# Kernel tuning notes

Measured on AMD Instinct MI355X. Metric: run time of the kernel, lower is better.

## Reference

```python
import jax, jax.numpy as jnp
import numpy as np

B, H, W, R, C = 4, 64, 64, 64, 32  # batch, height, width, in-channels r, conv out-channels


def setup_inputs() -> dict:
    key = jax.random.key(0)
    kx, kf, kg = jax.random.split(key, 3)
    x = jax.random.normal(kx, (B, H, W, R), dtype=jnp.float32)
    # 1x1 conv with in_channels=1: kernel is effectively a length-C vector
    w_f = jax.random.normal(kf, (C,), dtype=jnp.float32) * 0.1
    w_g = jax.random.normal(kg, (C,), dtype=jnp.float32) * 0.1
    gamma = jnp.ones((), dtype=jnp.float32)
    return {"x": x, "w_f": w_f, "w_g": w_g, "gamma": gamma}


def reference(x, w_f, w_g, gamma):
    b, h, w, r = x.shape
    hw = h * w
    xs = x.reshape(b, hw, r)                      # [B, HW, R]
    # conv_f / conv_g: each scalar of xs times weight vector -> [B, HW, R*C]
    x_f = (xs[..., None] * w_f).reshape(b, hw, -1)
    x_g = (xs[..., None] * w_g).reshape(b, hw, -1)
    attn = jnp.einsum('bik,bjk->bij', x_f, x_g)   # [B, HW, HW]
    attn = jax.nn.softmax(attn, axis=-1) * gamma
    # out[b,j,r] = sum_i attn[b,j,i] * xs[b,i,r]
    out = jnp.einsum('bji,bir->bjr', attn, xs)
    return out.reshape(b, h, w, r)
```

## Files before the change

### kernel.cpp

```cpp
#include <hip/hip_runtime.h>


#define N_SEQ 4096
#define LOG2E 1.4426950408889634f

typedef __attribute__((ext_vector_type(8))) short short8;
typedef __attribute__((ext_vector_type(4))) short short4v;
typedef __attribute__((ext_vector_type(4))) float f4;
typedef __attribute__((ext_vector_type(16))) float f32x16;
typedef _Float16 half8  __attribute__((ext_vector_type(8)));
typedef _Float16 half2t __attribute__((ext_vector_type(2)));
typedef __fp16   fp16x2 __attribute__((ext_vector_type(2)));

union U8  { short8 v8; short4v v4[2]; unsigned short u[8]; };
union PKU { fp16x2 f; half2t h; unsigned int u; };
union US  { short8 s; half8 h; };
union W4U { unsigned int u[4]; half8 h; };

#define MFMA16(a,b,c)  __builtin_amdgcn_mfma_f32_16x16x32_bf16(a,b,c,0,0,0)
#define MFMA32F(a,b,c) __builtin_amdgcn_mfma_f32_32x32x16_f16(a,b,c,0,0,0)

static __device__ __forceinline__ unsigned short f2bf(float f){
  unsigned int u = __float_as_uint(f);
  u += 0x7fffu + ((u>>16)&1u);
  return (unsigned short)(u>>16);
}
static __device__ __forceinline__ float bf2f(unsigned short b){
  return __uint_as_float(((unsigned int)b)<<16);
}
static __device__ __forceinline__ unsigned int pk_u32(float a, float b){
#if __has_builtin(__builtin_amdgcn_cvt_pkrtz)
  PKU u; u.f = __builtin_amdgcn_cvt_pkrtz(a, b); return u.u;
#else
  PKU u; u.h.x = (_Float16)a; u.h.y = (_Float16)b; return u.u;
#endif
}
static __device__ __forceinline__ float fexp2(float x){
#if __has_builtin(__builtin_amdgcn_exp2f)
  return __builtin_amdgcn_exp2f(x);
#else
  return exp2f(x);
#endif
}
static __device__ __forceinline__ f4 splat4(float v){ f4 r; r.x=v; r.y=v; r.z=v; r.w=v; return r; }
static __device__ __forceinline__ f4 exp2v(f4 v){
  f4 r; r.x=fexp2(v.x); r.y=fexp2(v.y); r.z=fexp2(v.z); r.w=fexp2(v.w); return r;
}
static __device__ __forceinline__ f4 max4(f4 a, f4 b){
  f4 r; r.x=fmaxf(a.x,b.x); r.y=fmaxf(a.y,b.y); r.z=fmaxf(a.z,b.z); r.w=fmaxf(a.w,b.w); return r;
}
static __device__ __forceinline__ f4 shx4(f4 v, int m){
  f4 r; r.x=__shfl_xor(v.x,m,64); r.y=__shfl_xor(v.y,m,64);
        r.z=__shfl_xor(v.z,m,64); r.w=__shfl_xor(v.w,m,64); return r;
}
static __device__ __forceinline__ f32x16 zero16(){
  f32x16 z;
  #pragma unroll
  for (int i = 0; i < 16; ++i) z[i] = 0.f;
  return z;
}
static __device__ __forceinline__ void gload16(const unsigned short* g, unsigned short* l){
  __builtin_amdgcn_global_load_lds((const __attribute__((address_space(1))) void*)g,
                                   (__attribute__((address_space(3))) void*)l, 16, 0, 0);
}
static __device__ __forceinline__ half8 mkfrag(unsigned int Da0, unsigned int Da1,
                                               unsigned int Db0, unsigned int Db1, bool hib){
  const unsigned int e0 = __shfl_xor(hib ? Da0 : Db0, 32, 64);
  const unsigned int e1 = __shfl_xor(hib ? Da1 : Db1, 32, 64);
  W4U w;
  w.u[0] = hib ? e0  : Da0;
  w.u[1] = hib ? e1  : Da1;
  w.u[2] = hib ? Db0 : e0;
  w.u[3] = hib ? Db1 : e1;
  return w.h;
}

__global__ __launch_bounds__(256) void prep6_kernel(
    const float* __restrict__ x,
    unsigned short* __restrict__ XF, unsigned short* __restrict__ VF)
{
  __shared__ __align__(16) unsigned short T [64][82];
  __shared__ __align__(16) unsigned short TT[64][82];
  const int tid  = threadIdx.x;
  const int bb   = blockIdx.x >> 6;
  const int tile = blockIdx.x & 63;
  {
    const int r  = tid >> 2;
    const int c4 = tid & 3;
    const float* src = x + ((size_t)(bb*N_SEQ + tile*64 + r))*64 + c4*16;
    unsigned short h[16];
    #pragma unroll
    for (int i = 0; i < 4; ++i) {
      const float4 f = *(const float4*)(src + i*4);
      const unsigned int u0 = pk_u32(f.x, f.y);
      const unsigned int u1 = pk_u32(f.z, f.w);
      h[i*4+0] = (unsigned short)(u0 & 0xffffu);
      h[i*4+1] = (unsigned short)(u0 >> 16);
      h[i*4+2] = (unsigned short)(u1 & 0xffffu);
      h[i*4+3] = (unsigned short)(u1 >> 16);
    }
    #pragma unroll
    for (int j = 0; j < 16; ++j) T[r][c4*16+j] = h[j];
    #pragma unroll
    for (int j = 0; j < 16; ++j) TT[c4*16+j][r] = h[j];
  }
  __syncthreads();
  const size_t ob = ((size_t)(bb*64 + tile)) * 4096;
  #pragma unroll
  for (int s0 = 0; s0 < 2; ++s0) {
    const int s  = s0*256 + tid;
    const int fb = s >> 6;
    const int l  = s & 63;
    const int rr = (fb >> 2)*32 + (l & 31);
    const int cc = (fb & 3)*16 + (l >> 5)*8;
    U8 a, b;
    #pragma unroll
    for (int j = 0; j < 8; ++j) { a.u[j] = T[rr][cc+j]; b.u[j] = TT[rr][cc+j]; }
    *(short8*)(XF + ob + (size_t)s*8) = a.v8;
    *(short8*)(VF + ob + (size_t)s*8) = b.v8;
  }
}

__global__ __launch_bounds__(512, 2) void fattn9_kernel(
    const float* __restrict__ wf, const float* __restrict__ wg,
    const float* __restrict__ gm,
    const unsigned short* __restrict__ XF, const unsigned short* __restrict__ VF,
    float* __restrict__ out)
{
  __shared__ __align__(16) unsigned char SMEM[66560];
  unsigned short* TLE  = (unsigned short*)SMEM;
  float*          LO   = (float*)SMEM;
  float*          LSUM = (float*)(SMEM + 65536);

  const int tid  = threadIdx.x;
  const int lane = tid & 63;
  const int wv   = tid >> 6;
  const int l31  = lane & 31;
  const int hi   = lane >> 5;
  const bool hib = hi != 0;
  const int par  = wv >> 2;
  const int kg   = (wv >> 1) & 1;
  const int qg   = wv & 1;
  const int bb   = blockIdx.x >> 6;
  const int qt   = blockIdx.x & 63;

  float s = 0.f;
  #pragma unroll
  for (int i = 0; i < 32; ++i) s += wf[i]*wg[i];
  const float s2 = s * LOG2E;
  const _Float16 s2h = (_Float16)s2;

  half8 qf[4];
  {
    const unsigned short* xq = XF + ((size_t)(bb*64 + qt))*4096 + lane*8;
    half8 sv;
    #pragma unroll
    for (int j = 0; j < 8; ++j) sv[j] = s2h;
    #pragma unroll
    for (int kst = 0; kst < 4; ++kst) {
      US u; u.s = *(const short8*)(xq + (qg*4+kst)*512);
      qf[kst] = u.h * sv;
    }
  }

  f32x16 Oc[2];
  Oc[0] = zero16(); Oc[1] = zero16();
  float lacc = 0.f;

  const unsigned short* gK = XF + (size_t)bb*64*4096;
  const unsigned short* gV = VF + (size_t)bb*64*4096;

  #define STAGE(p, b)                                                            \
    _Pragma("unroll")                                                            \
    for (int c = 0; c < 4; ++c) {                                                \
      const unsigned short* src =                                                \
        ((c >> 1) ? gV : gK) + ((size_t)((p)*2 + (c & 1)))*4096 + tid*8;         \
      unsigned short* dst = TLE + ((((b)*2 + (c & 1))*2 + (c >> 1))*4096) + tid*8;\
      gload16(src, dst);                                                         \
    }

  STAGE(0, 0);
  __syncthreads();

  #pragma unroll 1
  for (int it = 0; it < 32; ++it) {
    const int cur = it & 1;
    if (it + 1 < 32) { STAGE(it + 1, cur ^ 1); }

    const unsigned short* KB = TLE + ((cur*2 + par)*2 + 0)*4096;
    const unsigned short* VB = KB + 4096;

    half8 kf[4];
    #pragma unroll
    for (int kst = 0; kst < 4; ++kst) {
      US u; u.s = *(const short8*)(KB + ((kg*4+kst)*64 + lane)*8);
      kf[kst] = u.h;
    }
    f32x16 St = zero16();
    __builtin_amdgcn_s_setprio(1);
    #pragma unroll
    for (int kst = 0; kst < 4; ++kst) St = MFMA32F(kf[kst], qf[kst], St);
    __builtin_amdgcn_s_setprio(0);

    float p[16];
    float sm = 0.f;
    #pragma unroll
    for (int r = 0; r < 16; ++r) { p[r] = fexp2(St[r]); sm += p[r]; }
    lacc += sm;
    const unsigned int D0 = pk_u32(p[0],  p[1]);
    const unsigned int D1 = pk_u32(p[2],  p[3]);
    const unsigned int D2 = pk_u32(p[4],  p[5]);
    const unsigned int D3 = pk_u32(p[6],  p[7]);
    const unsigned int D4 = pk_u32(p[8],  p[9]);
    const unsigned int D5 = pk_u32(p[10], p[11]);
    const unsigned int D6 = pk_u32(p[12], p[13]);
    const unsigned int D7 = pk_u32(p[14], p[15]);
    half8 pa0 = mkfrag(D0, D1, D2, D3, hib);
    half8 pa1 = mkfrag(D4, D5, D6, D7, hib);

    __builtin_amdgcn_s_setprio(1);
    #pragma unroll
    for (int dg = 0; dg < 2; ++dg) {
      US v0, v1;
      v0.s = *(const short8*)(VB + ((dg*4 + kg*2 + 0)*64 + lane)*8);
      v1.s = *(const short8*)(VB + ((dg*4 + kg*2 + 1)*64 + lane)*8);
      Oc[dg] = MFMA32F(pa0, v0.h, Oc[dg]);
      Oc[dg] = MFMA32F(pa1, v1.h, Oc[dg]);
    }
    __builtin_amdgcn_s_setprio(0);

    __syncthreads();
  }

  lacc += __shfl_xor(lacc, 32, 64);

  #pragma unroll
  for (int dg = 0; dg < 2; ++dg)
    #pragma unroll
    for (int r = 0; r < 16; ++r) {
      const int ql = (r & 3) + 8*(r >> 2) + 4*hi;
      LO[wv*2048 + ql*64 + dg*32 + l31] = Oc[dg][r];
    }
  if (hi == 0) LSUM[wv*32 + l31] = lacc;
  __syncthreads();

  {
    const float gamma = gm[0];
    const int r  = tid >> 3;
    const int d0 = (tid & 7)*8;
    const int q  = r & 31;
    const int qr = r >> 5;
    const float l = LSUM[(qr+0)*32 + q] + LSUM[(qr+2)*32 + q]
                  + LSUM[(qr+4)*32 + q] + LSUM[(qr+6)*32 + q];
    const float w = gamma / l;
    float acc[8];
    #pragma unroll
    for (int j = 0; j < 8; ++j) acc[j] = 0.f;
    #pragma unroll
    for (int j = 0; j < 4; ++j) {
      const float* src = LO + (qr + j*2)*2048 + q*64 + d0;
      #pragma unroll
      for (int e = 0; e < 8; ++e) acc[e] += src[e];
    }
    float4 r0, r1;
    r0.x = acc[0]*w; r0.y = acc[1]*w; r0.z = acc[2]*w; r0.w = acc[3]*w;
    r1.x = acc[4]*w; r1.y = acc[5]*w; r1.z = acc[6]*w; r1.w = acc[7]*w;
    float* dst = out + ((size_t)(bb*N_SEQ + qt*64 + r))*64 + d0;
    *(float4*)dst = r0;
    *(float4*)(dst + 4) = r1;
  }
}

#define LDKF 72
#define TILEF (64*LDKF)
#define LDP 36

__global__ __launch_bounds__(256) void fattn_fallback(
    const float* __restrict__ x, const float* __restrict__ wf,
    const float* __restrict__ wg, const float* __restrict__ gm,
    float* __restrict__ out)
{
  __shared__ __align__(16) unsigned short KHI[2*TILEF];
  __shared__ __align__(16) unsigned short KLO[2*TILEF];
  __shared__ __align__(16) unsigned short VT [2*TILEF];
  __shared__ __align__(16) unsigned short PB [4*32*LDP];

  const int tid  = threadIdx.x;
  const int lane = tid & 63;
  const int wv   = tid >> 6;
  const int mg   = wv & 1;
  const int hh   = wv >> 1;
  const int quad = lane >> 4;
  const int l15  = lane & 15;
  const int bb   = blockIdx.x >> 6;
  const int qb   = (blockIdx.x & 63) << 6;

  float s = 0.f;
  #pragma unroll
  for (int i = 0; i < 32; ++i) s += wf[i]*wg[i];
  const float s2 = s * LOG2E;
  const float gamma = gm[0];

  const float* xb = x + ((size_t)bb * N_SEQ) * 64;

  short8 qhf[2][2], qlf[2][2];
  #pragma unroll
  for (int mt = 0; mt < 2; ++mt) {
    const int row = qb + mg*32 + mt*16 + l15;
    #pragma unroll
    for (int c = 0; c < 2; ++c) {
      const float* src = xb + row*64 + c*32 + quad*8;
      const float4 a0 = *(const float4*)src;
      const float4 a1 = *(const float4*)(src+4);
      float qv[8] = {a0.x,a0.y,a0.z,a0.w,a1.x,a1.y,a1.z,a1.w};
      U8 vh, vl;
      #pragma unroll
      for (int j = 0; j < 8; ++j) {
        float q = qv[j]*s2;
        unsigned short hb = f2bf(q);
        vh.u[j] = (short)hb;
        vl.u[j] = (short)f2bf(q - bf2f(hb));
      }
      qhf[mt][c] = vh.v8; qlf[mt][c] = vl.v8;
    }
  }

  f4 Oc[2][4], mo[2], ls[2];
  #pragma unroll
  for (int mt = 0; mt < 2; ++mt) {
    mo[mt] = splat4(-1e30f);
    ls[mt] = splat4(0.f);
    #pragma unroll
    for (int nt = 0; nt < 4; ++nt) Oc[mt][nt] = splat4(0.f);
  }

  const int sh   = tid >> 7;
  const int srow = (tid & 127) >> 1;
  const int sch  = tid & 1;

  float4 sr[8];
  {
    const float* sp = xb + (sh*2048 + srow)*64 + sch*32;
    #pragma unroll
    for (int i = 0; i < 8; ++i) sr[i] = *(const float4*)(sp + i*4);
    unsigned short hb[32], lb[32];
    #pragma unroll
    for (int i = 0; i < 8; ++i) {
      float vv[4] = {sr[i].x, sr[i].y, sr[i].z, sr[i].w};
      #pragma unroll
      for (int j = 0; j < 4; ++j) {
        unsigned short h = f2bf(vv[j]);
        hb[i*4+j] = h;
        lb[i*4+j] = f2bf(vv[j] - bf2f(h));
      }
    }
    const int kbase = sh*TILEF + srow*LDKF + sch*32;
    #pragma unroll
    for (int g = 0; g < 4; ++g) {
      U8 wh, wl;
      #pragma unroll
      for (int j = 0; j < 8; ++j) { wh.u[j]=(short)hb[g*8+j]; wl.u[j]=(short)lb[g*8+j]; }
      *(short8*)&KHI[kbase+g*8] = wh.v8;
      *(short8*)&KLO[kbase+g*8] = wl.v8;
    }
    #pragma unroll
    for (int j = 0; j < 32; ++j) VT[sh*TILEF + (sch*32+j)*LDKF + srow] = hb[j];
  }
  __syncthreads();

  #pragma unroll 1
  for (int t = 0; t < 32; ++t) {
    if (t+1 < 32) {
      const float* sp = xb + (sh*2048 + (t+1)*64 + srow)*64 + sch*32;
      #pragma unroll
      for (int i = 0; i < 8; ++i) sr[i] = *(const float4*)(sp + i*4);
    }

    f4 Sa[2][4];
    #pragma unroll
    for (int mt = 0; mt < 2; ++mt)
      #pragma unroll
      for (int n = 0; n < 4; ++n) Sa[mt][n] = splat4(0.f);

    const int kldsb = hh*TILEF;
    #pragma unroll
    for (int n = 0; n < 4; ++n) {
      #pragma unroll
      for (int c = 0; c < 2; ++c) {
        const int off = kldsb + (n*16 + l15)*LDKF + c*32 + quad*8;
        const short8 bh = *(const short8*)&KHI[off];
        const short8 bl = *(const short8*)&KLO[off];
        #pragma unroll
        for (int mt = 0; mt < 2; ++mt) {
          Sa[mt][n] = MFMA16(qhf[mt][c], bh, Sa[mt][n]);
          Sa[mt][n] = MFMA16(qlf[mt][c], bh, Sa[mt][n]);
          Sa[mt][n] = MFMA16(qhf[mt][c], bl, Sa[mt][n]);
        }
      }
    }

    f4 p[2][4];
    #pragma unroll
    for (int mt = 0; mt < 2; ++mt) {
      f4 rm = max4(max4(Sa[mt][0],Sa[mt][1]), max4(Sa[mt][2],Sa[mt][3]));
      rm = max4(rm, shx4(rm,1));
      rm = max4(rm, shx4(rm,2));
      rm = max4(rm, shx4(rm,4));
      rm = max4(rm, shx4(rm,8));
      f4 mn = max4(mo[mt], rm);
      f4 al = exp2v(mo[mt] - mn);
      mo[mt] = mn;
      f4 rs = splat4(0.f);
      #pragma unroll
      for (int n = 0; n < 4; ++n) { p[mt][n] = exp2v(Sa[mt][n] - mn); rs += p[mt][n]; }
      rs += shx4(rs,1); rs += shx4(rs,2); rs += shx4(rs,4); rs += shx4(rs,8);
      ls[mt] = ls[mt]*al + rs;
      #pragma unroll
      for (int nt = 0; nt < 4; ++nt) Oc[mt][nt] *= al;
    }

    const int pw = wv * (32*LDP);
    #pragma unroll
    for (int kc = 0; kc < 2; ++kc) {
      #pragma unroll
      for (int mt = 0; mt < 2; ++mt) {
        #pragma unroll
        for (int n2 = 0; n2 < 2; ++n2) {
          const f4 pv = p[mt][kc*2+n2];
          const int base = pw + (mt*16 + quad*4)*LDP + n2*16 + l15;
          ((unsigned short*)PB)[base        ] = f2bf(pv.x);
          ((unsigned short*)PB)[base +   LDP] = f2bf(pv.y);
          ((unsigned short*)PB)[base + 2*LDP] = f2bf(pv.z);
          ((unsigned short*)PB)[base + 3*LDP] = f2bf(pv.w);
        }
      }
      short8 pa[2];
      #pragma unroll
      for (int mt = 0; mt < 2; ++mt) {
        U8 u;
        const int rb = pw + (mt*16 + l15)*LDP + quad*8;
        u.v4[0] = *(const short4v*)&((unsigned short*)PB)[rb];
        u.v4[1] = *(const short4v*)&((unsigned short*)PB)[rb+4];
        pa[mt] = u.v8;
      }
      #pragma unroll
      for (int nt = 0; nt < 4; ++nt) {
        const short8 vb = *(const short8*)&VT[kldsb + (nt*16 + l15)*LDKF + kc*32 + quad*8];
        #pragma unroll
        for (int mt = 0; mt < 2; ++mt) Oc[mt][nt] = MFMA16(pa[mt], vb, Oc[mt][nt]);
      }
    }

    __syncthreads();

    if (t+1 < 32) {
      unsigned short hb[32], lb[32];
      #pragma unroll
      for (int i = 0; i < 8; ++i) {
        float vv[4] = {sr[i].x, sr[i].y, sr[i].z, sr[i].w};
        #pragma unroll
        for (int j = 0; j < 4; ++j) {
          unsigned short h = f2bf(vv[j]);
          hb[i*4+j] = h;
          lb[i*4+j] = f2bf(vv[j] - bf2f(h));
        }
      }
      const int kbase = sh*TILEF + srow*LDKF + sch*32;
      #pragma unroll
      for (int g = 0; g < 4; ++g) {
        U8 wh, wl;
        #pragma unroll
        for (int j = 0; j < 8; ++j) { wh.u[j]=(short)hb[g*8+j]; wl.u[j]=(short)lb[g*8+j]; }
        *(short8*)&KHI[kbase+g*8] = wh.v8;
        *(short8*)&KLO[kbase+g*8] = wl.v8;
      }
      #pragma unroll
      for (int j = 0; j < 32; ++j) VT[sh*TILEF + (sch*32+j)*LDKF + srow] = hb[j];
      __syncthreads();
    }
  }

  float* MO  = (float*)KHI;
  float* MML = (float*)KLO;
  if (hh == 1) {
    #pragma unroll
    for (int mt = 0; mt < 2; ++mt) {
      const int rbase = mg*32 + mt*16 + quad*4;
      #pragma unroll
      for (int nt = 0; nt < 4; ++nt) {
        MO[(rbase+0)*64 + nt*16 + l15] = Oc[mt][nt].x;
        MO[(rbase+1)*64 + nt*16 + l15] = Oc[mt][nt].y;
        MO[(rbase+2)*64 + nt*16 + l15] = Oc[mt][nt].z;
        MO[(rbase+3)*64 + nt*16 + l15] = Oc[mt][nt].w;
      }
      if (l15 == 0) {
        MML[rbase+0] = mo[mt].x; MML[rbase+1] = mo[mt].y;
        MML[rbase+2] = mo[mt].z; MML[rbase+3] = mo[mt].w;
        MML[64+rbase+0] = ls[mt].x; MML[64+rbase+1] = ls[mt].y;
        MML[64+rbase+2] = ls[mt].z; MML[64+rbase+3] = ls[mt].w;
      }
    }
  }
  __syncthreads();
  if (hh == 0) {
    #pragma unroll
    for (int mt = 0; mt < 2; ++mt) {
      const int rbase = mg*32 + mt*16 + quad*4;
      f4 m1, l1;
      m1.x = MML[rbase+0]; m1.y = MML[rbase+1]; m1.z = MML[rbase+2]; m1.w = MML[rbase+3];
      l1.x = MML[64+rbase+0]; l1.y = MML[64+rbase+1]; l1.z = MML[64+rbase+2]; l1.w = MML[64+rbase+3];
      const f4 mn = max4(mo[mt], m1);
      const f4 a0 = exp2v(mo[mt] - mn);
      const f4 a1 = exp2v(m1 - mn);
      f4 lt = ls[mt]*a0 + l1*a1;
      f4 w; w.x = gamma/lt.x; w.y = gamma/lt.y; w.z = gamma/lt.z; w.w = gamma/lt.w;
      #pragma unroll
      for (int nt = 0; nt < 4; ++nt) {
        #pragma unroll
        for (int rg = 0; rg < 4; ++rg) {
          const int rr = rbase + rg;
          const float o1 = MO[rr*64 + nt*16 + l15];
          const float val = (Oc[mt][nt][rg]*a0[rg] + o1*a1[rg]) * w[rg];
          out[((size_t)bb*N_SEQ + qb + rr)*64 + nt*16 + l15] = val;
        }
      }
    }
  }
}

extern "C" void kernel_launch(void* const* d_in, const int* in_sizes, int n_in,
                              void* d_out, int out_size, void* d_ws, size_t ws_size,
                              hipStream_t stream) {
  const float* x  = (const float*)d_in[0];
  const float* wf = (const float*)d_in[1];
  const float* wg = (const float*)d_in[2];
  const float* gm = (const float*)d_in[3];
  float* out = (float*)d_out;

  const size_t XF_OFF = 0;
  const size_t VF_OFF = 2097152;
  const size_t NEED   = 4194304;

  if (ws_size >= NEED) {
    unsigned short* XFp = (unsigned short*)((char*)d_ws + XF_OFF);
    unsigned short* VFp = (unsigned short*)((char*)d_ws + VF_OFF);
    prep6_kernel<<<dim3(256), dim3(256), 0, stream>>>(x, XFp, VFp);
    fattn9_kernel<<<dim3(256), dim3(512), 0, stream>>>(wf, wg, gm, XFp, VFp, out);
  } else {
    fattn_fallback<<<dim3(256), dim3(256), 0, stream>>>(x, wf, wg, gm, out);
  }
}
```

Measured before the change: 97.51 us.

## Give each wave both query halves and stage four KV tiles per iteration

```diff
diff --git a/kernel.cpp b/kernel.cpp
--- a/kernel.cpp
+++ b/kernel.cpp
@@ -121,16 +121,16 @@
   }
 }
 
-__global__ __launch_bounds__(512, 2) void fattn9_kernel(
+__global__ __launch_bounds__(512, 2) void fattn10_kernel(
     const float* __restrict__ wf, const float* __restrict__ wg,
     const float* __restrict__ gm,
     const unsigned short* __restrict__ XF, const unsigned short* __restrict__ VF,
     float* __restrict__ out)
 {
-  __shared__ __align__(16) unsigned char SMEM[66560];
+  __shared__ __align__(16) unsigned char SMEM[133120];
   unsigned short* TLE  = (unsigned short*)SMEM;
   float*          LO   = (float*)SMEM;
-  float*          LSUM = (float*)(SMEM + 65536);
+  float*          LSUM = (float*)(SMEM + 131072);
 
   const int tid  = threadIdx.x;
   const int lane = tid & 63;
@@ -138,9 +138,8 @@
   const int l31  = lane & 31;
   const int hi   = lane >> 5;
   const bool hib = hi != 0;
-  const int par  = wv >> 2;
-  const int kg   = (wv >> 1) & 1;
-  const int qg   = wv & 1;
+  const int tp   = wv >> 1;
+  const int kg   = wv & 1;
   const int bb   = blockIdx.x >> 6;
   const int qt   = blockIdx.x & 63;
 
@@ -150,45 +149,48 @@
   const float s2 = s * LOG2E;
   const _Float16 s2h = (_Float16)s2;
 
-  half8 qf[4];
+  half8 qf[2][4];
   {
     const unsigned short* xq = XF + ((size_t)(bb*64 + qt))*4096 + lane*8;
     half8 sv;
     #pragma unroll
     for (int j = 0; j < 8; ++j) sv[j] = s2h;
     #pragma unroll
-    for (int kst = 0; kst < 4; ++kst) {
-      US u; u.s = *(const short8*)(xq + (qg*4+kst)*512);
-      qf[kst] = u.h * sv;
-    }
-  }
-
-  f32x16 Oc[2];
-  Oc[0] = zero16(); Oc[1] = zero16();
-  float lacc = 0.f;
+    for (int qg = 0; qg < 2; ++qg)
+      #pragma unroll
+      for (int kst = 0; kst < 4; ++kst) {
+        US u; u.s = *(const short8*)(xq + (qg*4+kst)*512);
+        qf[qg][kst] = u.h * sv;
+      }
+  }
+
+  f32x16 Oc[2][2];
+  #pragma unroll
+  for (int qg = 0; qg < 2; ++qg) { Oc[qg][0] = zero16(); Oc[qg][1] = zero16(); }
+  float lacc[2] = {0.f, 0.f};
 
   const unsigned short* gK = XF + (size_t)bb*64*4096;
   const unsigned short* gV = VF + (size_t)bb*64*4096;
 
-  #define STAGE(p, b)                                                            \
+  #define STAGE10(g, b)                                                          \
     _Pragma("unroll")                                                            \
-    for (int c = 0; c < 4; ++c) {                                                \
+    for (int c = 0; c < 8; ++c) {                                                \
       const unsigned short* src =                                                \
-        ((c >> 1) ? gV : gK) + ((size_t)((p)*2 + (c & 1)))*4096 + tid*8;         \
-      unsigned short* dst = TLE + ((((b)*2 + (c & 1))*2 + (c >> 1))*4096) + tid*8;\
+        ((c >> 2) ? gV : gK) + ((size_t)((g)*4 + (c & 3)))*4096 + tid*8;         \
+      unsigned short* dst = TLE + ((b)*8 + c)*4096 + tid*8;                      \
       gload16(src, dst);                                                         \
     }
 
-  STAGE(0, 0);
+  STAGE10(0, 0);
   __syncthreads();
 
   #pragma unroll 1
-  for (int it = 0; it < 32; ++it) {
+  for (int it = 0; it < 16; ++it) {
     const int cur = it & 1;
-    if (it + 1 < 32) { STAGE(it + 1, cur ^ 1); }
-
-    const unsigned short* KB = TLE + ((cur*2 + par)*2 + 0)*4096;
-    const unsigned short* VB = KB + 4096;
+    if (it + 1 < 16) { STAGE10(it + 1, cur ^ 1); }
+
+    const unsigned short* KB = TLE + (cur*8 + tp)*4096;
+    const unsigned short* VB = TLE + (cur*8 + 4 + tp)*4096;
 
     half8 kf[4];
     #pragma unroll
@@ -196,27 +198,35 @@
       US u; u.s = *(const short8*)(KB + ((kg*4+kst)*64 + lane)*8);
       kf[kst] = u.h;
     }
-    f32x16 St = zero16();
+    f32x16 St[2];
+    St[0] = zero16(); St[1] = zero16();
     __builtin_amdgcn_s_setprio(1);
     #pragma unroll
-    for (int kst = 0; kst < 4; ++kst) St = MFMA32F(kf[kst], qf[kst], St);
+    for (int kst = 0; kst < 4; ++kst) {
+      St[0] = MFMA32F(kf[kst], qf[0][kst], St[0]);
+      St[1] = MFMA32F(kf[kst], qf[1][kst], St[1]);
+    }
     __builtin_amdgcn_s_setprio(0);
 
-    float p[16];
-    float sm = 0.f;
-    #pragma unroll
-    for (int r = 0; r < 16; ++r) { p[r] = fexp2(St[r]); sm += p[r]; }
-    lacc += sm;
-    const unsigned int D0 = pk_u32(p[0],  p[1]);
-    const unsigned int D1 = pk_u32(p[2],  p[3]);
-    const unsigned int D2 = pk_u32(p[4],  p[5]);
-    const unsigned int D3 = pk_u32(p[6],  p[7]);
-    const unsigned int D4 = pk_u32(p[8],  p[9]);
-    const unsigned int D5 = pk_u32(p[10], p[11]);
-    const unsigned int D6 = pk_u32(p[12], p[13]);
-    const unsigned int D7 = pk_u32(p[14], p[15]);
-    half8 pa0 = mkfrag(D0, D1, D2, D3, hib);
-    half8 pa1 = mkfrag(D4, D5, D6, D7, hib);
+    half8 pa[2][2];
+    #pragma unroll
+    for (int qg = 0; qg < 2; ++qg) {
+      float p[16];
+      float sm = 0.f;
+      #pragma unroll
+      for (int r = 0; r < 16; ++r) { p[r] = fexp2(St[qg][r]); sm += p[r]; }
+      lacc[qg] += sm;
+      const unsigned int D0 = pk_u32(p[0],  p[1]);
+      const unsigned int D1 = pk_u32(p[2],  p[3]);
+      const unsigned int D2 = pk_u32(p[4],  p[5]);
+      const unsigned int D3 = pk_u32(p[6],  p[7]);
+      const unsigned int D4 = pk_u32(p[8],  p[9]);
+      const unsigned int D5 = pk_u32(p[10], p[11]);
+      const unsigned int D6 = pk_u32(p[12], p[13]);
+      const unsigned int D7 = pk_u32(p[14], p[15]);
+      pa[qg][0] = mkfrag(D0, D1, D2, D3, hib);
+      pa[qg][1] = mkfrag(D4, D5, D6, D7, hib);
+    }
 
     __builtin_amdgcn_s_setprio(1);
     #pragma unroll
@@ -224,47 +234,54 @@
       US v0, v1;
       v0.s = *(const short8*)(VB + ((dg*4 + kg*2 + 0)*64 + lane)*8);
       v1.s = *(const short8*)(VB + ((dg*4 + kg*2 + 1)*64 + lane)*8);
-      Oc[dg] = MFMA32F(pa0, v0.h, Oc[dg]);
-      Oc[dg] = MFMA32F(pa1, v1.h, Oc[dg]);
+      #pragma unroll
+      for (int qg = 0; qg < 2; ++qg) {
+        Oc[qg][dg] = MFMA32F(pa[qg][0], v0.h, Oc[qg][dg]);
+        Oc[qg][dg] = MFMA32F(pa[qg][1], v1.h, Oc[qg][dg]);
+      }
     }
     __builtin_amdgcn_s_setprio(0);
 
     __syncthreads();
   }
 
-  lacc += __shfl_xor(lacc, 32, 64);
-
-  #pragma unroll
-  for (int dg = 0; dg < 2; ++dg)
-    #pragma unroll
-    for (int r = 0; r < 16; ++r) {
-      const int ql = (r & 3) + 8*(r >> 2) + 4*hi;
-      LO[wv*2048 + ql*64 + dg*32 + l31] = Oc[dg][r];
-    }
-  if (hi == 0) LSUM[wv*32 + l31] = lacc;
+  lacc[0] += __shfl_xor(lacc[0], 32, 64);
+  lacc[1] += __shfl_xor(lacc[1], 32, 64);
+
+  #pragma unroll
+  for (int qg = 0; qg < 2; ++qg) {
+    #pragma unroll
+    for (int dg = 0; dg < 2; ++dg)
+      #pragma unroll
+      for (int r = 0; r < 16; ++r) {
+        const int ql = qg*32 + (r & 3) + 8*(r >> 2) + 4*hi;
+        LO[wv*4096 + ql*64 + dg*32 + l31] = Oc[qg][dg][r];
+      }
+    if (hi == 0) LSUM[wv*64 + qg*32 + l31] = lacc[qg];
+  }
   __syncthreads();
 
   {
     const float gamma = gm[0];
     const int r  = tid >> 3;
     const int d0 = (tid & 7)*8;
-    const int q  = r & 31;
-    const int qr = r >> 5;
-    const float l = LSUM[(qr+0)*32 + q] + LSUM[(qr+2)*32 + q]
-                  + LSUM[(qr+4)*32 + q] + LSUM[(qr+6)*32 + q];
-    const float w = gamma / l;
+    float l = 0.f;
+    #pragma unroll
+    for (int w = 0; w < 8; ++w) l += LSUM[w*64 + r];
+    const float wgt = gamma / l;
     float acc[8];
     #pragma unroll
     for (int j = 0; j < 8; ++j) acc[j] = 0.f;
     #pragma unroll
-    for (int j = 0; j < 4; ++j) {
-      const float* src = LO + (qr + j*2)*2048 + q*64 + d0;
-      #pragma unroll
-      for (int e = 0; e < 8; ++e) acc[e] += src[e];
+    for (int w = 0; w < 8; ++w) {
+      const float4 a0 = *(const float4*)(LO + w*4096 + r*64 + d0);
+      const float4 a1 = *(const float4*)(LO + w*4096 + r*64 + d0 + 4);
+      acc[0] += a0.x; acc[1] += a0.y; acc[2] += a0.z; acc[3] += a0.w;
+      acc[4] += a1.x; acc[5] += a1.y; acc[6] += a1.z; acc[7] += a1.w;
     }
     float4 r0, r1;
-    r0.x = acc[0]*w; r0.y = acc[1]*w; r0.z = acc[2]*w; r0.w = acc[3]*w;
-    r1.x = acc[4]*w; r1.y = acc[5]*w; r1.z = acc[6]*w; r1.w = acc[7]*w;
+    r0.x = acc[0]*wgt; r0.y = acc[1]*wgt; r0.z = acc[2]*wgt; r0.w = acc[3]*wgt;
+    r1.x = acc[4]*wgt; r1.y = acc[5]*wgt; r1.z = acc[6]*wgt; r1.w = acc[7]*wgt;
     float* dst = out + ((size_t)(bb*N_SEQ + qt*64 + r))*64 + d0;
     *(float4*)dst = r0;
     *(float4*)(dst + 4) = r1;
@@ -545,7 +562,7 @@
     unsigned short* XFp = (unsigned short*)((char*)d_ws + XF_OFF);
     unsigned short* VFp = (unsigned short*)((char*)d_ws + VF_OFF);
     prep6_kernel<<<dim3(256), dim3(256), 0, stream>>>(x, XFp, VFp);
-    fattn9_kernel<<<dim3(256), dim3(512), 0, stream>>>(wf, wg, gm, XFp, VFp, out);
+    fattn10_kernel<<<dim3(256), dim3(512), 0, stream>>>(wf, wg, gm, XFp, VFp, out);
   } else {
     fattn_fallback<<<dim3(256), dim3(256), 0, stream>>>(x, wf, wg, gm, out);
   }
```

Result: faster. 94.00 us (-3.6%).
